# Performance work log

Hardware: AMD Instinct MI355X
Metric: run time of the kernel (lower is better)

Reference implementation:

```python
import jax, jax.numpy as jnp
import numpy as np

NCE_T = 0.07


def setup_inputs() -> dict:
    key = jax.random.key(0)
    k1, k2, k3 = jax.random.split(key, 3)
    features_1 = jax.random.normal(k1, (1, 20000, 256), dtype=jnp.float32)
    features_2 = jax.random.normal(k2, (1, 8192, 256), dtype=jnp.float32)
    map21 = jax.random.randint(k3, (8192,), 0, 20000, dtype=jnp.int64)
    return {"features_1": features_1, "features_2": features_2, "map21": map21}


def reference(features_1, features_2, map21):
    # squeeze leading batch dim (module assumes batch size 1)
    f1 = features_1[0]  # [N1, D]
    f2 = features_2[0]  # [P, D]  (P == nce_num_pairs == len(map21) -> arange branch)
    query = f1[map21]   # [P, D] gather
    keys = f2           # [P, D]
    # pairwise Euclidean distance via matmul trick (matches torch.cdist p=2)
    q_sq = jnp.sum(query * query, axis=-1)  # [P]
    k_sq = jnp.sum(keys * keys, axis=-1)    # [P]
    sq_dist = q_sq[:, None] + k_sq[None, :] - 2.0 * (query @ keys.T)  # [P, P]
    dist = jnp.sqrt(jnp.maximum(sq_dist, 0.0))
    logits = -dist / NCE_T
    # cross entropy with labels = arange(P): mean of -log_softmax diagonal
    logp = jax.nn.log_softmax(logits, axis=-1)
    loss = -jnp.mean(jnp.diagonal(logp))
    return loss
```

## Files before the change

kernel.cpp:

```cpp
#include <hip/hip_runtime.h>
#include <hip/hip_bf16.h>

#define PP      8192
#define DIM     256
#define DIMP    272
#define NKF     17
#define GS      (32 * DIMP)
#define NCHUNK  16
#define TCOLS   16
#define ROWBLK  256
#define NROWBLK (PP / ROWBLK)
#define TILEB   (32 * DIMP * 2)
#define NBUF    4

typedef __bf16 bf16_t;
using bf16x8 = __attribute__((ext_vector_type(8))) __bf16;
using bf16x4 = __attribute__((ext_vector_type(4))) __bf16;
using f32x4  = __attribute__((ext_vector_type(4))) float;
using f32x16 = __attribute__((ext_vector_type(16))) float;

typedef __attribute__((address_space(1))) void as1_void;
typedef __attribute__((address_space(3))) void as3_void;

#define C2    20.609929155556618
#define MEXP  (-340.0f)
#define COEF  ((float)(-(C2 * 1.4142135623730951) * 8388608.0))
#define KBIAS ((float)((127.0 + 340.0) * 8388608.0))
#define LN2   0.6931471805599453f

__global__ __launch_bounds__(256) void nce_prep(
    const float* __restrict__ f1, const float* __restrict__ f2,
    const int* __restrict__ map,
    bf16_t* __restrict__ qb2, bf16_t* __restrict__ kb2,
    float* __restrict__ diag2, float* __restrict__ part_l,
    unsigned* __restrict__ cnt, float* __restrict__ out)
{
    const int tid  = threadIdx.x;
    const int wave = tid >> 6, lane = tid & 63;
    const int p    = blockIdx.x * 4 + wave;
    const int gtid = blockIdx.x * 256 + tid;

    if (gtid < PP) part_l[gtid] = 0.0f;
    if (gtid < NROWBLK) cnt[gtid] = 0u;
    if (gtid == 0) out[0] = 0.0f;

    const int idx = map[p];
    const f32x4 qv = *(const f32x4*)(f1 + (size_t)idx * DIM + lane * 4);
    const f32x4 kv = *(const f32x4*)(f2 + (size_t)p * DIM + lane * 4);

    float qs = qv[0]*qv[0] + qv[1]*qv[1] + qv[2]*qv[2] + qv[3]*qv[3];
    float ks = kv[0]*kv[0] + kv[1]*kv[1] + kv[2]*kv[2] + kv[3]*kv[3];
    const f32x4 dv = qv - kv;
    float ds = dv[0]*dv[0] + dv[1]*dv[1] + dv[2]*dv[2] + dv[3]*dv[3];

    bf16x4 qo, ko;
    #pragma unroll
    for (int i = 0; i < 4; ++i) { qo[i] = (bf16_t)qv[i]; ko[i] = (bf16_t)kv[i]; }

    const int G = p >> 5, l31 = p & 31;
    const int kk = lane >> 2, h = (lane >> 1) & 1, j0 = (lane & 1) * 4;
    const size_t base = (size_t)G * GS;
    const size_t off  = base + (size_t)(kk * 64 + h * 32 + l31) * 8 + j0;
    *(bf16x4*)(qb2 + off) = qo;
    *(bf16x4*)(kb2 + off) = ko;

    #pragma unroll
    for (int s = 32; s > 0; s >>= 1) {
        qs += __shfl_xor(qs, s);
        ks += __shfl_xor(ks, s);
        ds += __shfl_xor(ds, s);
    }

    if (lane < 4) {
        const int hh = lane & 1;
        bf16x8 v;
        #pragma unroll
        for (int i = 0; i < 8; ++i) v[i] = (bf16_t)0.0f;
        if (lane == 0) {
            const float qh = -0.5f * qs;
            const bf16_t q1 = (bf16_t)qh;
            v[0] = q1; v[1] = (bf16_t)(qh - (float)q1);
            v[2] = (bf16_t)1.0f; v[3] = (bf16_t)1.0f;
        } else if (lane == 2) {
            const float kh = -0.5f * ks;
            const bf16_t k1 = (bf16_t)kh;
            v[0] = (bf16_t)1.0f; v[1] = (bf16_t)1.0f;
            v[2] = k1; v[3] = (bf16_t)(kh - (float)k1);
        }
        bf16_t* dstp = (lane < 2) ? qb2 : kb2;
        *(bf16x8*)(dstp + base + (size_t)(1024 + hh * 32 + l31) * 8) = v;
    }
    if (lane == 0)
        diag2[p] = (float)(-C2) * __builtin_amdgcn_sqrtf(ds);
}

__device__ __forceinline__ void stage(const bf16_t* __restrict__ kb2,
                                      int Gc, int wave, int lane, char* dst)
{
    __builtin_assume(wave >= 0 && wave < 4);
    __builtin_assume(lane >= 0 && lane < 64);
    const bf16_t* src = kb2 + (size_t)Gc * GS + wave * 512 + lane * 8;
    char* d = dst + wave * 1024;
    #pragma unroll
    for (int j = 0; j < 4; ++j)
        __builtin_amdgcn_global_load_lds((const as1_void*)(src + j * 2048),
                                         (as3_void*)(d + j * 4096), 16, 0, 0);
    if (wave == 0)
        __builtin_amdgcn_global_load_lds((const as1_void*)(src + 4 * 2048),
                                         (as3_void*)(d + 4 * 4096), 16, 0, 0);
}

#define PHASE(NW, DOPRE, T)                                                    \
  do {                                                                         \
    asm volatile("s_waitcnt vmcnt(%c0) lgkmcnt(0)\n\ts_barrier"                \
                 :: "i"(NW) : "memory");                                       \
    if (DOPRE) {                                                               \
        stage(kb2, c0g + (T) + 3, wave, lane, smem[((T) + 3) & 3]);            \
        __builtin_amdgcn_sched_barrier(0x7);           \
    }                                                                          \
    const bf16_t* bp = (const bf16_t*)smem[(T) & 3] + lane * 8;                \
    f32x16 acc0 = {0,0,0,0,0,0,0,0,0,0,0,0,0,0,0,0};                          \
    f32x16 acc1 = {0,0,0,0,0,0,0,0,0,0,0,0,0,0,0,0};                          \
    __builtin_amdgcn_s_setprio(1);                                             \
    _Pragma("unroll")                                                          \
    for (int kk = 0; kk < NKF; ++kk) {                                         \
        const bf16x8 b = *(const bf16x8*)(bp + kk * 512);                      \
        acc0 = __builtin_amdgcn_mfma_f32_32x32x16_bf16(a0[kk], b, acc0,0,0,0); \
        acc1 = __builtin_amdgcn_mfma_f32_32x32x16_bf16(a1[kk], b, acc1,0,0,0); \
    }                                                                          \
    __builtin_amdgcn_s_setprio(0);                                             \
         \
    _Pragma("unroll")                                                          \
    for (int i = 0; i < 16; ++i) {                                             \
        const float t0 = __builtin_amdgcn_sqrtf(-acc0[i]);                     \
        const float u0 = fmaxf(fmaf(t0, COEF, KBIAS), 0.0f);                   \
        l0[i] += __uint_as_float((unsigned)u0);                                \
        const float t1 = __builtin_amdgcn_sqrtf(-acc1[i]);                     \
        const float u1 = fmaxf(fmaf(t1, COEF, KBIAS), 0.0f);                   \
        l1[i] += __uint_as_float((unsigned)u1);                                \
    }                                                                          \
  } while (0)

__global__ __launch_bounds__(256, 2) void nce_main(
    const bf16_t* __restrict__ qb2, const bf16_t* __restrict__ kb2,
    const float* __restrict__ diag2, float* __restrict__ part_l,
    unsigned* __restrict__ cnt, float* __restrict__ out)
{
    const int tid  = threadIdx.x, wave = tid >> 6, lane = tid & 63;
    const int l31  = lane & 31, h = lane >> 5;
    const int rb   = blockIdx.x;
    const int G0   = rb * 8 + wave * 2;
    const int c0g  = blockIdx.y * TCOLS;

    __shared__ __align__(16) char smem[NBUF][TILEB];
    __shared__ int s_last;

    stage(kb2, c0g + 0, wave, lane, smem[0]);
    stage(kb2, c0g + 1, wave, lane, smem[1]);
    stage(kb2, c0g + 2, wave, lane, smem[2]);

    bf16x8 a0[NKF], a1[NKF];
    {
        const bf16_t* ap0 = qb2 + (size_t)G0 * GS + lane * 8;
        const bf16_t* ap1 = ap0 + GS;
        #pragma unroll
        for (int kk = 0; kk < NKF; ++kk) {
            a0[kk] = *(const bf16x8*)(ap0 + kk * 512);
            a1[kk] = *(const bf16x8*)(ap1 + kk * 512);
        }
    }

    float l0[16], l1[16];
    #pragma unroll
    for (int i = 0; i < 16; ++i) { l0[i] = 0.0f; l1[i] = 0.0f; }

    #pragma unroll 1
    for (int t = 0; t < 13; ++t)
        PHASE(8, true, t);
    PHASE(8, false, 13);
    PHASE(4, false, 14);
    PHASE(0, false, 15);

    #pragma unroll
    for (int s = 1; s < 32; s <<= 1) {
        #pragma unroll
        for (int i = 0; i < 16; ++i) {
            l0[i] += __shfl_xor(l0[i], s);
            l1[i] += __shfl_xor(l1[i], s);
        }
    }

    if (l31 == 0) {
        #pragma unroll
        for (int i = 0; i < 16; ++i) {
            const int r = (i & 3) + 8 * (i >> 2) + 4 * h;
            atomicAdd(&part_l[G0 * 32 + r], l0[i]);
            atomicAdd(&part_l[(G0 + 1) * 32 + r], l1[i]);
        }
    }

    __syncthreads();
    if (tid == 0) {
        __threadfence();
        s_last = (atomicAdd(&cnt[rb], 1u) == NCHUNK - 1) ? 1 : 0;
    }
    __syncthreads();
    if (s_last) {
        const int row = rb * ROWBLK + tid;
        const float lf = atomicAdd(&part_l[row], 0.0f);
        float v = MEXP + __builtin_amdgcn_logf(lf) - diag2[row];
        #pragma unroll
        for (int s = 1; s < 64; s <<= 1) v += __shfl_xor(v, s);
        __shared__ float red[4];
        if (lane == 0) red[wave] = v;
        __syncthreads();
        if (tid == 0)
            atomicAdd(out, (red[0] + red[1] + red[2] + red[3]) * (LN2 / (float)PP));
    }
}

extern "C" void kernel_launch(void* const* d_in, const int* in_sizes, int n_in,
                              void* d_out, int out_size, void* d_ws, size_t ws_size,
                              hipStream_t stream)
{
    const float* f1  = (const float*)d_in[0];
    const float* f2  = (const float*)d_in[1];
    const int*   map = (const int*)d_in[2];
    float* out = (float*)d_out;

    char* ws = (char*)d_ws;
    bf16_t*   qb2    = (bf16_t*)ws;
    bf16_t*   kb2    = qb2 + (size_t)256 * GS;
    float*    diag2  = (float*)(ws + 2ull * 256 * GS * sizeof(bf16_t));
    float*    part_l = diag2 + PP;
    unsigned* cnt    = (unsigned*)(part_l + PP);

    nce_prep<<<PP / 4, 256, 0, stream>>>(f1, f2, map, qb2, kb2, diag2,
                                         part_l, cnt, out);
    nce_main<<<dim3(NROWBLK, NCHUNK), 256, 0, stream>>>(qb2, kb2, diag2,
                                                        part_l, cnt, out);
}
```

Measured before the change: 118.2 us.

## Halve per-wave row tiles, double-buffer LDS, raise occupancy and remap blocks per XCD

Result: slower. 128.0 us (+8.3%).

```diff
diff --git a/kernel.cpp b/kernel.cpp
--- a/kernel.cpp
+++ b/kernel.cpp
@@ -8,10 +8,10 @@
 #define GS      (32 * DIMP)
 #define NCHUNK  16
 #define TCOLS   16
-#define ROWBLK  256
+#define ROWBLK  128
 #define NROWBLK (PP / ROWBLK)
 #define TILEB   (32 * DIMP * 2)
-#define NBUF    4
+#define NBUF    2
 
 typedef __bf16 bf16_t;
 using bf16x8 = __attribute__((ext_vector_type(8))) __bf16;
@@ -112,90 +112,77 @@
 
 #define PHASE(NW, DOPRE, T)                                                    \
   do {                                                                         \
-    asm volatile("s_waitcnt vmcnt(%c0) lgkmcnt(0)\n\ts_barrier"                \
-                 :: "i"(NW) : "memory");                                       \
-    if (DOPRE) {                                                               \
-        stage(kb2, c0g + (T) + 3, wave, lane, smem[((T) + 3) & 3]);            \
-        __builtin_amdgcn_sched_barrier(0x7);           \
-    }                                                                          \
-    const bf16_t* bp = (const bf16_t*)smem[(T) & 3] + lane * 8;                \
-    f32x16 acc0 = {0,0,0,0,0,0,0,0,0,0,0,0,0,0,0,0};                          \
-    f32x16 acc1 = {0,0,0,0,0,0,0,0,0,0,0,0,0,0,0,0};                          \
+    asm volatile("s_waitcnt lgkmcnt(0)\n\ts_barrier" ::: "memory");            \
+    if (DOPRE) stage(kb2, c0g + (T) + 1, wave, lane, smem[((T) + 1) & 1]);     \
+    asm volatile("s_waitcnt vmcnt(%c0)" :: "i"(NW) : "memory");                \
+    const bf16_t* bp = (const bf16_t*)smem[(T) & 1] + lane * 8;                \
+    f32x16 acc = {0,0,0,0,0,0,0,0,0,0,0,0,0,0,0,0};                           \
     __builtin_amdgcn_s_setprio(1);                                             \
     _Pragma("unroll")                                                          \
     for (int kk = 0; kk < NKF; ++kk) {                                         \
         const bf16x8 b = *(const bf16x8*)(bp + kk * 512);                      \
-        acc0 = __builtin_amdgcn_mfma_f32_32x32x16_bf16(a0[kk], b, acc0,0,0,0); \
-        acc1 = __builtin_amdgcn_mfma_f32_32x32x16_bf16(a1[kk], b, acc1,0,0,0); \
+        acc = __builtin_amdgcn_mfma_f32_32x32x16_bf16(a[kk], b, acc, 0, 0, 0); \
     }                                                                          \
     __builtin_amdgcn_s_setprio(0);                                             \
          \
     _Pragma("unroll")                                                          \
     for (int i = 0; i < 16; ++i) {                                             \
-        const float t0 = __builtin_amdgcn_sqrtf(-acc0[i]);                     \
-        const float u0 = fmaxf(fmaf(t0, COEF, KBIAS), 0.0f);                   \
-        l0[i] += __uint_as_float((unsigned)u0);                                \
-        const float t1 = __builtin_amdgcn_sqrtf(-acc1[i]);                     \
-        const float u1 = fmaxf(fmaf(t1, COEF, KBIAS), 0.0f);                   \
-        l1[i] += __uint_as_float((unsigned)u1);                                \
+        const float tt = __builtin_amdgcn_sqrtf(-acc[i]);                      \
+        const float uu = fmaxf(fmaf(tt, COEF, KBIAS), 0.0f);                   \
+        l[i] += __uint_as_float((unsigned)uu);                                 \
     }                                                                          \
   } while (0)
 
-__global__ __launch_bounds__(256, 2) void nce_main(
+__global__ __launch_bounds__(256, 4) void nce_main(
     const bf16_t* __restrict__ qb2, const bf16_t* __restrict__ kb2,
     const float* __restrict__ diag2, float* __restrict__ part_l,
     unsigned* __restrict__ cnt, float* __restrict__ out)
 {
     const int tid  = threadIdx.x, wave = tid >> 6, lane = tid & 63;
     const int l31  = lane & 31, h = lane >> 5;
-    const int rb   = blockIdx.x;
-    const int G0   = rb * 8 + wave * 2;
-    const int c0g  = blockIdx.y * TCOLS;
+
+    const int lin = blockIdx.x + (blockIdx.y << 6);
+    const int xcd = lin & 7, idx = lin >> 3;
+    const int rb  = (xcd & 3) * 16 + (idx & 15);
+    const int cy  = (xcd >> 2) * 8 + (idx >> 4);
+    const int G0  = rb * 4 + wave;
+    const int c0g = cy * TCOLS;
 
     __shared__ __align__(16) char smem[NBUF][TILEB];
     __shared__ int s_last;
-
-    stage(kb2, c0g + 0, wave, lane, smem[0]);
-    stage(kb2, c0g + 1, wave, lane, smem[1]);
-    stage(kb2, c0g + 2, wave, lane, smem[2]);
-
-    bf16x8 a0[NKF], a1[NKF];
+    __shared__ float red[4];
+
+    stage(kb2, c0g, wave, lane, smem[0]);
+
+    bf16x8 a[NKF];
     {
-        const bf16_t* ap0 = qb2 + (size_t)G0 * GS + lane * 8;
-        const bf16_t* ap1 = ap0 + GS;
-        #pragma unroll
-        for (int kk = 0; kk < NKF; ++kk) {
-            a0[kk] = *(const bf16x8*)(ap0 + kk * 512);
-            a1[kk] = *(const bf16x8*)(ap1 + kk * 512);
-        }
-    }
-
-    float l0[16], l1[16];
-    #pragma unroll
-    for (int i = 0; i < 16; ++i) { l0[i] = 0.0f; l1[i] = 0.0f; }
+        const bf16_t* ap = qb2 + (size_t)G0 * GS + lane * 8;
+        #pragma unroll
+        for (int kk = 0; kk < NKF; ++kk)
+            a[kk] = *(const bf16x8*)(ap + kk * 512);
+    }
+
+    float l[16];
+    #pragma unroll
+    for (int i = 0; i < 16; ++i) l[i] = 0.0f;
 
     #pragma unroll 1
-    for (int t = 0; t < 13; ++t)
-        PHASE(8, true, t);
-    PHASE(8, false, 13);
-    PHASE(4, false, 14);
-    PHASE(0, false, 15);
+    for (int t = 0; t < TCOLS - 1; ++t)
+        PHASE(4, true, t);
+    PHASE(0, false, TCOLS - 1);
 
     #pragma unroll
     for (int s = 1; s < 32; s <<= 1) {
         #pragma unroll
-        for (int i = 0; i < 16; ++i) {
-            l0[i] += __shfl_xor(l0[i], s);
-            l1[i] += __shfl_xor(l1[i], s);
-        }
+        for (int i = 0; i < 16; ++i)
+            l[i] += __shfl_xor(l[i], s);
     }
 
     if (l31 == 0) {
         #pragma unroll
         for (int i = 0; i < 16; ++i) {
             const int r = (i & 3) + 8 * (i >> 2) + 4 * h;
-            atomicAdd(&part_l[G0 * 32 + r], l0[i]);
-            atomicAdd(&part_l[(G0 + 1) * 32 + r], l1[i]);
+            atomicAdd(&part_l[G0 * 32 + r], l[i]);
         }
     }
 
@@ -206,12 +193,14 @@
     }
     __syncthreads();
     if (s_last) {
-        const int row = rb * ROWBLK + tid;
-        const float lf = atomicAdd(&part_l[row], 0.0f);
-        float v = MEXP + __builtin_amdgcn_logf(lf) - diag2[row];
+        float v = 0.0f;
+        if (tid < ROWBLK) {
+            const int row = rb * ROWBLK + tid;
+            const float lf = atomicAdd(&part_l[row], 0.0f);
+            v = MEXP + __builtin_amdgcn_logf(lf) - diag2[row];
+        }
         #pragma unroll
         for (int s = 1; s < 64; s <<= 1) v += __shfl_xor(v, s);
-        __shared__ float red[4];
         if (lane == 0) red[wave] = v;
         __syncthreads();
         if (tid == 0)
```
